# Performance work log

Measured on AMD Instinct MI355X. Metric: run time of the kernel, lower is better.

Reference implementation:

```python
import jax, jax.numpy as jnp
import numpy as np

B, T, C, L = 1024, 256, 128, 64
NEG = -1e30  # finite stand-in for -inf (safe gradients)
EPS = 1e-7   # keras.backend.epsilon()


def setup_inputs() -> dict:
    key = jax.random.key(0)
    k1, k2 = jax.random.split(key)
    # y_pred is a softmax output (probabilities), as keras ctc_batch_cost expects
    logits = jax.random.normal(k1, (B, T, C), dtype=jnp.float32)
    y_pred = jax.nn.softmax(logits, axis=-1)
    # labels in [0, C-2]; class C-1 is the CTC blank (keras convention)
    y_true = jax.random.randint(k2, (B, L), 0, C - 1, dtype=jnp.int64)
    return {"y_true": y_true, "y_pred": y_pred}


def ctc_loss(y_true, y_pred):
    """Negative log-likelihood CTC loss per sample, shape [B, 1].
    Matches keras.backend.ctc_batch_cost with full input/label lengths,
    blank index = num_classes - 1, log(y_pred + eps)."""
    Bb, Tt, Cc = y_pred.shape
    Ll = y_true.shape[1]
    blank = Cc - 1
    S = 2 * Ll + 1  # extended label: blank, l1, blank, l2, ..., blank

    logp = jnp.log(y_pred + EPS)  # [B, T, C]

    ext = jnp.full((Bb, S), blank, dtype=y_true.dtype).at[:, 1::2].set(y_true)  # [B, S]
    # per-(t, s) log-prob of the extended symbol: lp[b, t, s] = logp[b, t, ext[b, s]]
    lp = jnp.take_along_axis(logp, ext[:, None, :], axis=2)  # [B, T, S]

    # skip transition s-2 -> s allowed iff ext[s] != blank and ext[s] != ext[s-2]
    ext_m2 = jnp.concatenate(
        [jnp.full((Bb, 2), blank, dtype=ext.dtype), ext[:, :-2]], axis=1)
    can_skip = (ext != blank) & (ext != ext_m2)  # [B, S]

    def shift1(a):
        return jnp.concatenate(
            [jnp.full((Bb, 1), NEG, dtype=a.dtype), a[:, :-1]], axis=1)

    # alpha init at t=0: only s=0 (blank) and s=1 (first label) reachable
    alpha0 = (jnp.full((Bb, S), NEG, dtype=lp.dtype)
              .at[:, 0].set(lp[:, 0, 0])
              .at[:, 1].set(lp[:, 0, 1]))

    def step(alpha, lp_t):
        a1 = shift1(alpha)
        a2 = jnp.where(can_skip, shift1(shift1(alpha)), NEG)
        new = jax.nn.logsumexp(jnp.stack([alpha, a1, a2], axis=0), axis=0) + lp_t
        return new, None

    lp_tbs = jnp.swapaxes(lp, 0, 1)  # [T, B, S]
    alpha, _ = jax.lax.scan(step, alpha0, lp_tbs[1:])

    log_lik = jnp.logaddexp(alpha[:, S - 1], alpha[:, S - 2])  # end on last blank or last label
    return -log_lik[:, None]  # [B, 1], matching ctc_batch_cost output shape


def reference(y_true, y_pred):
    return ctc_loss(y_true, y_pred)
```

## Files before the change

### kernel.cpp

```cpp
#include <hip/hip_runtime.h>
#include <math.h>


#define Bn 1024
#define Tn 256
#define Cn 128
#define Ln 64
#define BLANK 127
#define U 8
#define NC (Tn / U)
#define RING 8
#define DEPTH 7
#define EPS128 (1e-7f * 128.0f)
#define LN2 0.69314718055994530942f

#define WAIT_VM(n) __builtin_amdgcn_s_waitcnt((((n) & 0xF) | (((n) >> 4) << 14)) | 0x0F70)
#define SCHED_FENCE() __builtin_amdgcn_sched_barrier(0)

template <int CTRL>
__device__ __forceinline__ float dpp_movf(float x) {
    return __int_as_float(__builtin_amdgcn_update_dpp(
        0, __float_as_int(x), CTRL, 0xF, 0xF, true));
}
__device__ __forceinline__ int dpp_shr1_i(int x) {
    return __builtin_amdgcn_update_dpp(0, x, 0x138, 0xF, 0xF, true);
}
__device__ __forceinline__ void dma16(const float* g, float* l) {
    __builtin_amdgcn_global_load_lds(
        (const __attribute__((address_space(1))) void*)g,
        (__attribute__((address_space(3))) void*)l, 16, 0, 0);
}

__global__ __launch_bounds__(64)
void ctc_ring_kernel(const int* __restrict__ y_true,
                     const float* __restrict__ y_pred,
                     float* __restrict__ out) {
    __shared__ __align__(16) float ring[RING][U * Cn];
    const int b = blockIdx.x;
    const int i = threadIdx.x;

    const int li = y_true[b * Ln + i];
    const int ll = dpp_shr1_i(li);
    const float skf = (li != ll) ? 1.0f : 0.0f;

    const float* gb = y_pred + (size_t)b * (Tn * Cn);

    auto issue_chunk = [&](int c) {
        const float* g = gb + c * (U * Cn);
        float* l = ring[c & (RING - 1)];
#pragma unroll
        for (int k = 0; k < 4; ++k)
            dma16(g + k * 256 + i * 4, l + k * 256);
    };

    float qlA[U], qbA[U], qlB[U], qbB[U];
    auto qread = [&](int c, float* ql, float* qb) {
        const float* s = ring[c & (RING - 1)];
#pragma unroll
        for (int j = 0; j < U; ++j) {
            ql[j] = fmaf(s[j * Cn + li],    128.0f, EPS128);
            qb[j] = fmaf(s[j * Cn + BLANK], 128.0f, EPS128);
        }
    };

    float E = 0.f, O = 0.f, X = 0.f;
    int Esum = 0;

    auto steps = [&](const float* ql, const float* qb, bool first) {
#pragma unroll
        for (int j = 0; j < U; ++j) {
            if (first && j == 0) {
                E = (i == 0) ? qb[0] : 0.f;
                O = (i == 0) ? ql[0] : 0.f;
                X = 0.f;
                continue;
            }
            const float Ol = dpp_movf<0x138>(O);
            const float t1 = O + E;
            const float nO = fmaf(skf, Ol, t1) * ql[j];
            const float nE = (E + Ol) * qb[j];
            const float nX = (X + O) * qb[j];
            E = nE; O = nO; X = nX;
        }
    };
    auto renorm = [&]() {
        float m = fmaxf(E, O);
        if (i == 63) m = fmaxf(m, X);
        m = fmaxf(m, dpp_movf<0x111>(m));
        m = fmaxf(m, dpp_movf<0x112>(m));
        m = fmaxf(m, dpp_movf<0x114>(m));
        m = fmaxf(m, dpp_movf<0x118>(m));
        m = fmaxf(m, dpp_movf<0x142>(m));
        m = fmaxf(m, dpp_movf<0x143>(m));
        const unsigned ub =
            (unsigned)__builtin_amdgcn_readlane(__float_as_int(m), 63);
        const int eb = (int)(ub >> 23);
        const float sc = __int_as_float((unsigned)(254 - eb) << 23);
        Esum += eb - 127;
        E *= sc; O *= sc; X *= sc;
    };

#pragma unroll
    for (int c = 0; c < DEPTH; ++c) issue_chunk(c);
    WAIT_VM(24);
    SCHED_FENCE();
    qread(0, qlA, qbA);

    for (int cc = 0; cc < 24; cc += 2) {
        WAIT_VM(20); SCHED_FENCE();
        qread(cc + 1, qlB, qbB);
        issue_chunk(cc + 7);
        steps(qlA, qbA, cc == 0);
        renorm();
        WAIT_VM(20); SCHED_FENCE();
        qread(cc + 2, qlA, qbA);
        issue_chunk(cc + 8);
        steps(qlB, qbB, false);
        renorm();
    }
    WAIT_VM(20); SCHED_FENCE();
    qread(25, qlB, qbB);
    issue_chunk(31);
    steps(qlA, qbA, false);
    renorm();
    WAIT_VM(0); SCHED_FENCE();
    qread(26, qlA, qbA);
    steps(qlB, qbB, false);
    renorm();
    qread(27, qlB, qbB); steps(qlA, qbA, false); renorm();
    qread(28, qlA, qbA); steps(qlB, qbB, false); renorm();
    qread(29, qlB, qbB); steps(qlA, qbA, false); renorm();
    qread(30, qlA, qbA); steps(qlB, qbB, false); renorm();
    qread(31, qlB, qbB); steps(qlA, qbA, false); renorm();
    steps(qlB, qbB, false);

    if (i == 63) {
        const float s = O + X;
#if __has_builtin(__builtin_amdgcn_logf)
        const float l2 = __builtin_amdgcn_logf(s);
#else
        const float l2 = log2f(s);
#endif
        out[b] = -(l2 + (float)(Esum - 7 * Tn)) * LN2;
    }
}

extern "C" void kernel_launch(void* const* d_in, const int* in_sizes, int n_in,
                              void* d_out, int out_size, void* d_ws, size_t ws_size,
                              hipStream_t stream) {
    const int*   y_true = (const int*)d_in[0];
    const float* y_pred = (const float*)d_in[1];
    float*       out    = (float*)d_out;
    hipLaunchKernelGGL(ctc_ring_kernel, dim3(Bn), dim3(64), 0, stream,
                       y_true, y_pred, out);
}
```

Baseline: 191.9 us.

## Split into a parallel gather/pack kernel and a compact bf16 recurrence kernel

A new pre-pass kernel reads each sample's full probability tensor with high parallelism, gathers only the per-label and blank probabilities, scales them, rounds to bf16 and writes a compact packed workspace. The recurrence kernel then DMAs about 34 KB per sample into LDS in one shot and runs the serial alpha recursion from local memory. This takes the 128 KB per-sample read off the single-wave serial critical path. The costs are a second launch, a workspace round trip, and lower bf16 precision on the probabilities.

```diff
diff --git a/kernel.cpp b/kernel.cpp
--- a/kernel.cpp
+++ b/kernel.cpp
@@ -8,9 +8,11 @@
 #define Ln 64
 #define BLANK 127
 #define U 8
-#define NC (Tn / U)
-#define RING 8
-#define DEPTH 7
+#define NCH (Tn / U)
+#define ENT 66
+#define CB (ENT * U * 2)
+#define WSB (NCH * CB)
+#define NLOAD (WSB / 1024)
 #define EPS128 (1e-7f * 128.0f)
 #define LN2 0.69314718055994530942f
 
@@ -25,41 +27,95 @@
 __device__ __forceinline__ int dpp_shr1_i(int x) {
     return __builtin_amdgcn_update_dpp(0, x, 0x138, 0xF, 0xF, true);
 }
-__device__ __forceinline__ void dma16(const float* g, float* l) {
+__device__ __forceinline__ void dma16(const void* g, void* l) {
     __builtin_amdgcn_global_load_lds(
         (const __attribute__((address_space(1))) void*)g,
         (__attribute__((address_space(3))) void*)l, 16, 0, 0);
 }
 
+__global__ __launch_bounds__(256)
+void ctc_pack_kernel(const int* __restrict__ yt,
+                     const float* __restrict__ yp,
+                     unsigned int* __restrict__ ws) {
+    const int b = blockIdx.y;
+    const int s = blockIdx.x;
+    const int w = threadIdx.x >> 6;
+    const int i = threadIdx.x & 63;
+
+    const int li    = yt[b * Ln + i];
+    const int baddr = (li >> 1) << 2;
+    const int sel   = li & 1;
+
+    const float2* rows = (const float2*)(yp + (size_t)b * (Tn * Cn)
+                                         + (size_t)(s * 64 + w * 16) * Cn);
+    float2 r[16];
+#pragma unroll
+    for (int t = 0; t < 16; ++t) r[t] = rows[t * (Cn / 2) + i];
+
+    unsigned qdw[2][4], bdw[2][4];
+#pragma unroll
+    for (int h = 0; h < 2; ++h)
+#pragma unroll
+        for (int k = 0; k < 4; ++k) { qdw[h][k] = 0u; bdw[h][k] = 0u; }
+
+#pragma unroll
+    for (int t = 0; t < 16; ++t) {
+        const float q0 = fmaf(r[t].x, 128.0f, EPS128);
+        const float q1 = fmaf(r[t].y, 128.0f, EPS128);
+        const unsigned u0 = __float_as_uint(q0), u1 = __float_as_uint(q1);
+        const unsigned c0 = (u0 + 0x7FFFu + ((u0 >> 16) & 1u)) >> 16;
+        const unsigned c1 = (u1 + 0x7FFFu + ((u1 >> 16) & 1u)) >> 16;
+        const unsigned pk = c0 | (c1 << 16);
+        const unsigned g  = (unsigned)__builtin_amdgcn_ds_bpermute(baddr, (int)pk);
+        const unsigned val = sel ? (g >> 16) : (g & 0xFFFFu);
+        const unsigned blk = ((unsigned)__builtin_amdgcn_readlane((int)pk, 63)) >> 16;
+        const int h = t >> 3, k = (t & 7) >> 1, sh = (t & 1) << 4;
+        qdw[h][k] |= val << sh;
+        bdw[h][k] |= blk << sh;
+    }
+
+    const int c0i = s * 8 + w * 2;
+#pragma unroll
+    for (int h = 0; h < 2; ++h) {
+        unsigned int* base = ws + ((size_t)b * WSB + (size_t)(c0i + h) * CB) / 4;
+        *(uint4*)(base + i * 4) =
+            make_uint4(qdw[h][0], qdw[h][1], qdw[h][2], qdw[h][3]);
+        if (i == 0)
+            *(uint4*)(base + 64 * 4) =
+                make_uint4(bdw[h][0], bdw[h][1], bdw[h][2], bdw[h][3]);
+    }
+}
+
 __global__ __launch_bounds__(64)
-void ctc_ring_kernel(const int* __restrict__ y_true,
-                     const float* __restrict__ y_pred,
-                     float* __restrict__ out) {
-    __shared__ __align__(16) float ring[RING][U * Cn];
+void ctc_rec_kernel(const int* __restrict__ yt,
+                    const unsigned int* __restrict__ ws,
+                    float* __restrict__ out) {
+    __shared__ __align__(16) unsigned int lds[WSB / 4];
+
     const int b = blockIdx.x;
     const int i = threadIdx.x;
 
-    const int li = y_true[b * Ln + i];
+    const int li = yt[b * Ln + i];
     const int ll = dpp_shr1_i(li);
     const float skf = (li != ll) ? 1.0f : 0.0f;
 
-    const float* gb = y_pred + (size_t)b * (Tn * Cn);
-
-    auto issue_chunk = [&](int c) {
-        const float* g = gb + c * (U * Cn);
-        float* l = ring[c & (RING - 1)];
+    const char* wsb = (const char*)(ws) + (size_t)b * WSB;
 #pragma unroll
-        for (int k = 0; k < 4; ++k)
-            dma16(g + k * 256 + i * 4, l + k * 256);
-    };
+    for (int k = 0; k < NLOAD; ++k)
+        dma16(wsb + k * 1024 + i * 16, (char*)lds + k * 1024);
 
     float qlA[U], qbA[U], qlB[U], qbB[U];
     auto qread = [&](int c, float* ql, float* qb) {
-        const float* s = ring[c & (RING - 1)];
+        const uint4 vq = *(const uint4*)((const char*)lds + c * CB + i * 16);
+        const uint4 vb = *(const uint4*)((const char*)lds + c * CB + 1024);
+        const unsigned q[4] = {vq.x, vq.y, vq.z, vq.w};
+        const unsigned bq[4] = {vb.x, vb.y, vb.z, vb.w};
 #pragma unroll
-        for (int j = 0; j < U; ++j) {
-            ql[j] = fmaf(s[j * Cn + li],    128.0f, EPS128);
-            qb[j] = fmaf(s[j * Cn + BLANK], 128.0f, EPS128);
+        for (int k = 0; k < 4; ++k) {
+            ql[2 * k]     = __uint_as_float(q[k] << 16);
+            ql[2 * k + 1] = __uint_as_float(q[k] & 0xFFFF0000u);
+            qb[2 * k]     = __uint_as_float(bq[k] << 16);
+            qb[2 * k + 1] = __uint_as_float(bq[k] & 0xFFFF0000u);
         }
     };
 
@@ -100,37 +156,19 @@
         E *= sc; O *= sc; X *= sc;
     };
 
-#pragma unroll
-    for (int c = 0; c < DEPTH; ++c) issue_chunk(c);
-    WAIT_VM(24);
-    SCHED_FENCE();
+    WAIT_VM(16); SCHED_FENCE();
     qread(0, qlA, qbA);
-
-    for (int cc = 0; cc < 24; cc += 2) {
-        WAIT_VM(20); SCHED_FENCE();
-        qread(cc + 1, qlB, qbB);
-        issue_chunk(cc + 7);
-        steps(qlA, qbA, cc == 0);
-        renorm();
-        WAIT_VM(20); SCHED_FENCE();
-        qread(cc + 2, qlA, qbA);
-        issue_chunk(cc + 8);
-        steps(qlB, qbB, false);
-        renorm();
+    for (int cc = 0; cc < 14; cc += 2) {
+        qread(cc + 1, qlB, qbB); steps(qlA, qbA, cc == 0); renorm();
+        qread(cc + 2, qlA, qbA); steps(qlB, qbB, false);   renorm();
     }
-    WAIT_VM(20); SCHED_FENCE();
-    qread(25, qlB, qbB);
-    issue_chunk(31);
-    steps(qlA, qbA, false);
-    renorm();
+    qread(15, qlB, qbB); steps(qlA, qbA, false); renorm();
     WAIT_VM(0); SCHED_FENCE();
-    qread(26, qlA, qbA);
-    steps(qlB, qbB, false);
-    renorm();
-    qread(27, qlB, qbB); steps(qlA, qbA, false); renorm();
-    qread(28, qlA, qbA); steps(qlB, qbB, false); renorm();
-    qread(29, qlB, qbB); steps(qlA, qbA, false); renorm();
-    qread(30, qlA, qbA); steps(qlB, qbB, false); renorm();
+    qread(16, qlA, qbA); steps(qlB, qbB, false); renorm();
+    for (int cc = 16; cc < 30; cc += 2) {
+        qread(cc + 1, qlB, qbB); steps(qlA, qbA, false); renorm();
+        qread(cc + 2, qlA, qbA); steps(qlB, qbB, false); renorm();
+    }
     qread(31, qlB, qbB); steps(qlA, qbA, false); renorm();
     steps(qlB, qbB, false);
 
@@ -151,6 +189,10 @@
     const int*   y_true = (const int*)d_in[0];
     const float* y_pred = (const float*)d_in[1];
     float*       out    = (float*)d_out;
-    hipLaunchKernelGGL(ctc_ring_kernel, dim3(Bn), dim3(64), 0, stream,
-                       y_true, y_pred, out);
+    unsigned int* ws    = (unsigned int*)d_ws;
+
+    hipLaunchKernelGGL(ctc_pack_kernel, dim3(4, Bn), dim3(256), 0, stream,
+                       y_true, y_pred, ws);
+    hipLaunchKernelGGL(ctc_rec_kernel, dim3(Bn), dim3(64), 0, stream,
+                       y_true, ws, out);
 }
```

Result: slower. 206.9 us (+7.8%).

## Split CTC kernel into producer/consumer warps with flag-synchronized LDS ring

Applied to the files above, without the earlier changes.

Replaces the single-wave design, which used direct global-to-LDS DMA with hand-tuned waitcnts, with a 256-thread block. Three producer waves load chunks through registers into an 8-slot LDS ring and publish per-chunk ready flags, while one consumer wave spins on those flags and runs the alpha recursion. The consumer reports its progress so producers never overwrite a slot still in use. This aims to take memory issue and latency off the serial recursion wave. In exchange it uses four times the threads per block, relies on volatile spin-wait synchronization, and has three of the four waves mostly sleeping.

```diff
diff --git a/kernel.cpp b/kernel.cpp
--- a/kernel.cpp
+++ b/kernel.cpp
@@ -8,14 +8,12 @@
 #define Ln 64
 #define BLANK 127
 #define U 8
-#define NC (Tn / U)
+#define NCH (Tn / U)
 #define RING 8
-#define DEPTH 7
 #define EPS128 (1e-7f * 128.0f)
 #define LN2 0.69314718055994530942f
 
-#define WAIT_VM(n) __builtin_amdgcn_s_waitcnt((((n) & 0xF) | (((n) >> 4) << 14)) | 0x0F70)
-#define SCHED_FENCE() __builtin_amdgcn_sched_barrier(0)
+#define WAIT_LGKM0() __builtin_amdgcn_s_waitcnt(0xC07F)
 
 template <int CTRL>
 __device__ __forceinline__ float dpp_movf(float x) {
@@ -25,35 +23,66 @@
 __device__ __forceinline__ int dpp_shr1_i(int x) {
     return __builtin_amdgcn_update_dpp(0, x, 0x138, 0xF, 0xF, true);
 }
-__device__ __forceinline__ void dma16(const float* g, float* l) {
-    __builtin_amdgcn_global_load_lds(
-        (const __attribute__((address_space(1))) void*)g,
-        (__attribute__((address_space(3))) void*)l, 16, 0, 0);
-}
 
-__global__ __launch_bounds__(64)
-void ctc_ring_kernel(const int* __restrict__ y_true,
-                     const float* __restrict__ y_pred,
-                     float* __restrict__ out) {
+__global__ __launch_bounds__(256)
+void ctc_pc_kernel(const int* __restrict__ yt,
+                   const float* __restrict__ yp,
+                   float* __restrict__ out) {
     __shared__ __align__(16) float ring[RING][U * Cn];
+    __shared__ int flags[NCH];
+    __shared__ int cons_prog;
+    volatile int* vfl = flags;
+    volatile int* vpr = &cons_prog;
+
     const int b = blockIdx.x;
-    const int i = threadIdx.x;
+    const int t = threadIdx.x;
+    const int w = t >> 6;
+    const int i = t & 63;
 
-    const int li = y_true[b * Ln + i];
+    if (t < NCH) flags[t] = 0;
+    if (t == 0)  cons_prog = 0;
+    __syncthreads();
+
+    const float* gb = yp + (size_t)b * (Tn * Cn);
+
+    if (w != 0) {
+        const int start = w - 1;
+        float4 fA[4], fB[4];
+        auto issue = [&](int c, float4* f) {
+            const float4* p = (const float4*)(gb + c * (U * Cn)) + i;
+#pragma unroll
+            for (int k = 0; k < 4; ++k) f[k] = p[k * 64];
+        };
+        auto put = [&](int c, const float4* f) {
+            while (*vpr < c - (RING - 1)) __builtin_amdgcn_s_sleep(1);
+            float4* d = (float4*)ring[c & (RING - 1)] + i;
+#pragma unroll
+            for (int k = 0; k < 4; ++k) d[k * 64] = f[k];
+            WAIT_LGKM0();
+            if (i == 0) vfl[c] = 1;
+        };
+        issue(start, fA);
+        if (start + 3 < NCH) issue(start + 3, fB);
+        for (int c = start; c < NCH; c += 6) {
+            put(c, fA);
+            if (c + 6 < NCH) issue(c + 6, fA);
+            if (c + 3 < NCH) {
+                put(c + 3, fB);
+                if (c + 9 < NCH) issue(c + 9, fB);
+            }
+        }
+        return;
+    }
+
+    const int li = yt[b * Ln + i];
     const int ll = dpp_shr1_i(li);
     const float skf = (li != ll) ? 1.0f : 0.0f;
 
-    const float* gb = y_pred + (size_t)b * (Tn * Cn);
-
-    auto issue_chunk = [&](int c) {
-        const float* g = gb + c * (U * Cn);
-        float* l = ring[c & (RING - 1)];
-#pragma unroll
-        for (int k = 0; k < 4; ++k)
-            dma16(g + k * 256 + i * 4, l + k * 256);
+    float qlA[U], qbA[U], qlB[U], qbB[U];
+    auto spinflag = [&](int c) {
+        while (vfl[c] == 0) __builtin_amdgcn_s_sleep(1);
+        __builtin_amdgcn_sched_barrier(0);
     };
-
-    float qlA[U], qbA[U], qlB[U], qbB[U];
     auto qread = [&](int c, float* ql, float* qb) {
         const float* s = ring[c & (RING - 1)];
 #pragma unroll
@@ -100,38 +129,25 @@
         E *= sc; O *= sc; X *= sc;
     };
 
-#pragma unroll
-    for (int c = 0; c < DEPTH; ++c) issue_chunk(c);
-    WAIT_VM(24);
-    SCHED_FENCE();
+    spinflag(0);
     qread(0, qlA, qbA);
-
-    for (int cc = 0; cc < 24; cc += 2) {
-        WAIT_VM(20); SCHED_FENCE();
-        qread(cc + 1, qlB, qbB);
-        issue_chunk(cc + 7);
-        steps(qlA, qbA, cc == 0);
+    for (int c = 0; c < NCH - 2; c += 2) {
+        spinflag(c + 1);
+        qread(c + 1, qlB, qbB);
+        steps(qlA, qbA, c == 0);
         renorm();
-        WAIT_VM(20); SCHED_FENCE();
-        qread(cc + 2, qlA, qbA);
-        issue_chunk(cc + 8);
+        if (i == 0) *vpr = c + 1;
+        spinflag(c + 2);
+        qread(c + 2, qlA, qbA);
         steps(qlB, qbB, false);
         renorm();
+        if (i == 0) *vpr = c + 2;
     }
-    WAIT_VM(20); SCHED_FENCE();
-    qread(25, qlB, qbB);
-    issue_chunk(31);
+    spinflag(NCH - 1);
+    qread(NCH - 1, qlB, qbB);
     steps(qlA, qbA, false);
     renorm();
-    WAIT_VM(0); SCHED_FENCE();
-    qread(26, qlA, qbA);
-    steps(qlB, qbB, false);
-    renorm();
-    qread(27, qlB, qbB); steps(qlA, qbA, false); renorm();
-    qread(28, qlA, qbA); steps(qlB, qbB, false); renorm();
-    qread(29, qlB, qbB); steps(qlA, qbA, false); renorm();
-    qread(30, qlA, qbA); steps(qlB, qbB, false); renorm();
-    qread(31, qlB, qbB); steps(qlA, qbA, false); renorm();
+    if (i == 0) *vpr = NCH - 1;
     steps(qlB, qbB, false);
 
     if (i == 63) {
@@ -151,6 +167,6 @@
     const int*   y_true = (const int*)d_in[0];
     const float* y_pred = (const float*)d_in[1];
     float*       out    = (float*)d_out;
-    hipLaunchKernelGGL(ctc_ring_kernel, dim3(Bn), dim3(64), 0, stream,
+    hipLaunchKernelGGL(ctc_pc_kernel, dim3(Bn), dim3(256), 0, stream,
                        y_true, y_pred, out);
 }
```

Measured after the change: 217.1 us. +13.2%, slower.

## Replace LDS DMA ring with register-held chunks and bpermute label gather

Applied to the files above, without the earlier changes.

Loads each timestep row directly into registers as float2 per lane instead of DMA'ing chunks into an LDS ring buffer. Label probabilities are gathered with ds_bpermute and the blank probability via readlane from lane 63. Loads are software-pipelined four chunks deep in registers, and renormalization now happens every two chunks instead of every chunk. This removes the LDS write/read round trip and explicit waitcnt management, at the cost of more registers, shallower prefetch, and larger dynamic range between renorms.

```diff
diff --git a/kernel.cpp b/kernel.cpp
--- a/kernel.cpp
+++ b/kernel.cpp
@@ -6,16 +6,10 @@
 #define Tn 256
 #define Cn 128
 #define Ln 64
-#define BLANK 127
 #define U 8
-#define NC (Tn / U)
-#define RING 8
-#define DEPTH 7
+#define NCH (Tn / U)
 #define EPS128 (1e-7f * 128.0f)
 #define LN2 0.69314718055994530942f
-
-#define WAIT_VM(n) __builtin_amdgcn_s_waitcnt((((n) & 0xF) | (((n) >> 4) << 14)) | 0x0F70)
-#define SCHED_FENCE() __builtin_amdgcn_sched_barrier(0)
 
 template <int CTRL>
 __device__ __forceinline__ float dpp_movf(float x) {
@@ -25,41 +19,43 @@
 __device__ __forceinline__ int dpp_shr1_i(int x) {
     return __builtin_amdgcn_update_dpp(0, x, 0x138, 0xF, 0xF, true);
 }
-__device__ __forceinline__ void dma16(const float* g, float* l) {
-    __builtin_amdgcn_global_load_lds(
-        (const __attribute__((address_space(1))) void*)g,
-        (__attribute__((address_space(3))) void*)l, 16, 0, 0);
+__device__ __forceinline__ float bpermf(int baddr, float v) {
+    return __int_as_float(__builtin_amdgcn_ds_bpermute(baddr, __float_as_int(v)));
 }
 
 __global__ __launch_bounds__(64)
-void ctc_ring_kernel(const int* __restrict__ y_true,
-                     const float* __restrict__ y_pred,
-                     float* __restrict__ out) {
-    __shared__ __align__(16) float ring[RING][U * Cn];
+void ctc_reg_kernel(const int* __restrict__ yt,
+                    const float* __restrict__ yp,
+                    float* __restrict__ out) {
     const int b = blockIdx.x;
     const int i = threadIdx.x;
 
-    const int li = y_true[b * Ln + i];
+    const int li = yt[b * Ln + i];
     const int ll = dpp_shr1_i(li);
     const float skf = (li != ll) ? 1.0f : 0.0f;
+    const int  baddr = (li >> 1) << 2;
+    const bool sel   = (li & 1) != 0;
 
-    const float* gb = y_pred + (size_t)b * (Tn * Cn);
+    const float2* gb = (const float2*)(yp + (size_t)b * (Tn * Cn));
 
-    auto issue_chunk = [&](int c) {
-        const float* g = gb + c * (U * Cn);
-        float* l = ring[c & (RING - 1)];
+    float2 R0[U], R1[U], R2[U], R3[U];
+    float qlA[U], qbA[U], qlB[U], qbB[U];
+
+    auto load = [&](int c, float2* r) {
+        const float2* p = gb + (size_t)c * (U * Cn / 2) + i;
 #pragma unroll
-        for (int k = 0; k < 4; ++k)
-            dma16(g + k * 256 + i * 4, l + k * 256);
+        for (int j = 0; j < U; ++j) r[j] = p[j * (Cn / 2)];
     };
-
-    float qlA[U], qbA[U], qlB[U], qbB[U];
-    auto qread = [&](int c, float* ql, float* qb) {
-        const float* s = ring[c & (RING - 1)];
+    auto conv = [&](const float2* r, float* ql, float* qb) {
 #pragma unroll
         for (int j = 0; j < U; ++j) {
-            ql[j] = fmaf(s[j * Cn + li],    128.0f, EPS128);
-            qb[j] = fmaf(s[j * Cn + BLANK], 128.0f, EPS128);
+            const float gx = bpermf(baddr, r[j].x);
+            const float gy = bpermf(baddr, r[j].y);
+            const float pv = sel ? gy : gx;
+            ql[j] = fmaf(pv, 128.0f, EPS128);
+            const float bk = __int_as_float(
+                __builtin_amdgcn_readlane(__float_as_int(r[j].y), 63));
+            qb[j] = fmaf(bk, 128.0f, EPS128);
         }
     };
 
@@ -100,39 +96,25 @@
         E *= sc; O *= sc; X *= sc;
     };
 
-#pragma unroll
-    for (int c = 0; c < DEPTH; ++c) issue_chunk(c);
-    WAIT_VM(24);
-    SCHED_FENCE();
-    qread(0, qlA, qbA);
+    load(0, R0); load(1, R1); load(2, R2); load(3, R3);
+    conv(R0, qlA, qbA);
 
-    for (int cc = 0; cc < 24; cc += 2) {
-        WAIT_VM(20); SCHED_FENCE();
-        qread(cc + 1, qlB, qbB);
-        issue_chunk(cc + 7);
+    for (int cc = 0; cc < NCH; cc += 4) {
+        conv(R1, qlB, qbB);
+        if (cc + 4 < NCH) load(cc + 4, R0);
         steps(qlA, qbA, cc == 0);
+        conv(R2, qlA, qbA);
+        if (cc + 5 < NCH) load(cc + 5, R1);
+        steps(qlB, qbB, false);
         renorm();
-        WAIT_VM(20); SCHED_FENCE();
-        qread(cc + 2, qlA, qbA);
-        issue_chunk(cc + 8);
+        conv(R3, qlB, qbB);
+        if (cc + 6 < NCH) load(cc + 6, R2);
+        steps(qlA, qbA, false);
+        if (cc + 4 < NCH) conv(R0, qlA, qbA);
+        if (cc + 7 < NCH) load(cc + 7, R3);
         steps(qlB, qbB, false);
         renorm();
     }
-    WAIT_VM(20); SCHED_FENCE();
-    qread(25, qlB, qbB);
-    issue_chunk(31);
-    steps(qlA, qbA, false);
-    renorm();
-    WAIT_VM(0); SCHED_FENCE();
-    qread(26, qlA, qbA);
-    steps(qlB, qbB, false);
-    renorm();
-    qread(27, qlB, qbB); steps(qlA, qbA, false); renorm();
-    qread(28, qlA, qbA); steps(qlB, qbB, false); renorm();
-    qread(29, qlB, qbB); steps(qlA, qbA, false); renorm();
-    qread(30, qlA, qbA); steps(qlB, qbB, false); renorm();
-    qread(31, qlB, qbB); steps(qlA, qbA, false); renorm();
-    steps(qlB, qbB, false);
 
     if (i == 63) {
         const float s = O + X;
@@ -151,6 +133,6 @@
     const int*   y_true = (const int*)d_in[0];
     const float* y_pred = (const float*)d_in[1];
     float*       out    = (float*)d_out;
-    hipLaunchKernelGGL(ctc_ring_kernel, dim3(Bn), dim3(64), 0, stream,
+    hipLaunchKernelGGL(ctc_reg_kernel, dim3(Bn), dim3(64), 0, stream,
                        y_true, y_pred, out);
 }
```

New measurement: 191.9 us. Within noise of the previous version (+0.0%).
